# Performance work log

Hardware: AMD Instinct MI355X
Metric: run time of the kernel (lower is better)

Reference implementation:

```python
import jax, jax.numpy as jnp
import numpy as np

B, S, H = 4, 1024, 1024
NH, HD = 16, 64
SCALE = 1.0 / np.sqrt(HD)
VERB_BIAS, ROOT_BIAS, SUFFIX_BIAS = 2.0, 1.5, 1.2
BIG = np.float32(1e9)


def setup_inputs() -> dict:
    key = jax.random.key(0)
    ks = jax.random.split(key, 10)
    inp = {
        "hidden_states": jax.random.normal(ks[0], (B, S, H), dtype=jnp.float32),
        "morpho_types": jax.random.randint(ks[1], (B, S), 0, 5, dtype=jnp.int32),
        # torch Linear: y = x @ W.T + b; store W already transposed as [in, out]
        "Wq": jax.random.normal(ks[2], (H, H), dtype=jnp.float32) * 0.02,
        "bq": jnp.zeros((H,), dtype=jnp.float32),
        "Wk": jax.random.normal(ks[3], (H, H), dtype=jnp.float32) * 0.02,
        "bk": jnp.zeros((H,), dtype=jnp.float32),
        "Wv": jax.random.normal(ks[4], (H, H), dtype=jnp.float32) * 0.02,
        "bv": jnp.zeros((H,), dtype=jnp.float32),
        "Wo": jax.random.normal(ks[5], (H, H), dtype=jnp.float32) * 0.02,
        "bo": jnp.zeros((H,), dtype=jnp.float32),
    }
    return inp


def _morpho_bias(morpho_types):
    """Vectorized equivalent of _create_morpho_bias_mask. Returns [B, S, S]
    (the torch version broadcasts the same bias over all heads)."""
    is_verb = morpho_types == 2                      # [B, S]
    pos = jnp.arange(S)
    dist = jnp.abs(pos[:, None] - pos[None, :])      # [S, S]
    # mask non-verb columns with a huge distance; argmin ties -> smallest j,
    # matching torch's argmin over ascending verb_positions
    dist_m = jnp.where(is_verb[:, None, :], dist[None], BIG)  # [B, S, S]
    nearest = jnp.argmin(dist_m, axis=-1)            # [B, S]
    has_verb = jnp.any(is_verb, axis=-1)             # [B]
    verb_term = VERB_BIAS * jax.nn.one_hot(nearest, S, dtype=jnp.float32)
    verb_term = verb_term * has_verb[:, None, None].astype(jnp.float32)
    col_bias = (ROOT_BIAS * 0.5) * (morpho_types == 0).astype(jnp.float32) \
             + (SUFFIX_BIAS * 0.3) * (morpho_types == 1).astype(jnp.float32)  # [B, S]
    return verb_term + col_bias[:, None, :]          # [B, S, S]


def reference(hidden_states, morpho_types, Wq, bq, Wk, bk, Wv, bv, Wo, bo):
    def proj(W, b):
        y = hidden_states @ W + b                    # [B, S, H]
        return y.reshape(B, S, NH, HD).transpose(0, 2, 1, 3)  # [B, NH, S, HD]

    q = proj(Wq, bq)
    k = proj(Wk, bk)
    v = proj(Wv, bv)

    scores = jnp.einsum('bhqd,bhkd->bhqk', q, k) * SCALE   # [B, NH, S, S]
    scores = scores + _morpho_bias(morpho_types)[:, None]  # broadcast heads

    attn = jax.nn.softmax(scores, axis=-1)
    out = jnp.einsum('bhqk,bhkd->bhqd', attn, v)           # [B, NH, S, HD]
    out = out.transpose(0, 2, 1, 3).reshape(B, S, H)
    return out @ Wo + bo
```

## Files before the change

### kernel.cpp

```cpp
#include <hip/hip_runtime.h>


#define QSCALE 0.18033688011112042f
#define CB0    1.0820212806667225f
#define CB1    0.5193702147200268f
#define VERB2  2.8853900817779268f

typedef float  f32x4   __attribute__((ext_vector_type(4)));
typedef short  s16x8   __attribute__((ext_vector_type(8)));
typedef unsigned short u16x4 __attribute__((ext_vector_type(4)));
typedef unsigned short u16x8 __attribute__((ext_vector_type(8)));

#if __has_builtin(__builtin_amdgcn_exp2f)
#define EXP2F(x) __builtin_amdgcn_exp2f(x)
#else
#define EXP2F(x) exp2f(x)
#endif

__device__ __forceinline__ unsigned short f2bf(float f) {
  union { float f; unsigned u; } a; a.f = f;
  unsigned r = a.u + 0x7fffu + ((a.u >> 16) & 1u);
  return (unsigned short)(r >> 16);
}

__device__ __forceinline__ void async16(const void* g, void* l) {
  __builtin_amdgcn_global_load_lds(
      (const __attribute__((address_space(1))) unsigned int*)g,
      (__attribute__((address_space(3))) unsigned int*)l, 16, 0, 0);
}

__global__ __launch_bounds__(256) void k_prep(
    const float* __restrict__ hs, unsigned short* __restrict__ hsb,
    const float* __restrict__ Wq, const float* __restrict__ Wk,
    const float* __restrict__ Wv, const float* __restrict__ Wo,
    unsigned short* __restrict__ Wt, const int* __restrict__ mt,
    float* __restrict__ colbias, int* __restrict__ nearest) {
  __shared__ float t[64 * 68];
  int bx = blockIdx.x, tid = threadIdx.x;
  if (bx < 2048) {
    int i = (bx * 256 + tid) * 8;
    float4 v0 = *(const float4*)(hs + i);
    float4 v1 = *(const float4*)(hs + i + 4);
    u16x8 o;
    o[0] = f2bf(v0.x); o[1] = f2bf(v0.y); o[2] = f2bf(v0.z); o[3] = f2bf(v0.w);
    o[4] = f2bf(v1.x); o[5] = f2bf(v1.y); o[6] = f2bf(v1.z); o[7] = f2bf(v1.w);
    *(u16x8*)(hsb + i) = o;
  } else if (bx < 3072) {
    int w = (bx - 2048) >> 8, tt = (bx - 2048) & 255;
    const float* W = (w == 0) ? Wq : (w == 1) ? Wk : (w == 2) ? Wv : Wo;
    unsigned short* Wd = Wt + (size_t)w * 1048576;
    int n0 = (tt & 15) * 64, k0 = (tt >> 4) * 64;
    int r = tid >> 2, c0 = (tid & 3) * 16;
    const float* src = &W[(k0 + r) * 1024 + n0 + c0];
    float4 a0 = *(const float4*)(src + 0);
    float4 a1 = *(const float4*)(src + 4);
    float4 a2 = *(const float4*)(src + 8);
    float4 a3 = *(const float4*)(src + 12);
    *(float4*)&t[r * 68 + c0 + 0]  = a0;
    *(float4*)&t[r * 68 + c0 + 4]  = a1;
    *(float4*)&t[r * 68 + c0 + 8]  = a2;
    *(float4*)&t[r * 68 + c0 + 12] = a3;
    __syncthreads();
    u16x8 o0, o1;
#pragma unroll
    for (int j = 0; j < 8; j++) {
      o0[j] = f2bf(t[(c0 + j) * 68 + r]);
      o1[j] = f2bf(t[(c0 + 8 + j) * 68 + r]);
    }
    *(u16x8*)&Wd[(n0 + r) * 1024 + k0 + c0]     = o0;
    *(u16x8*)&Wd[(n0 + r) * 1024 + k0 + c0 + 8] = o1;
  } else {
    int i = bx - 3072;
    int b = i >> 2;
    int* sm = (int*)t;
    for (int j = tid; j < 1024; j += 256) sm[j] = mt[b * 1024 + j];
    __syncthreads();
    int q = (i & 3) * 256 + tid;
    int best = 1 << 30, bj = -1;
    for (int j = 0; j < 1024; ++j) {
      int d = (q > j) ? (q - j) : (j - q);
      int dd = (sm[j] == 2) ? d : (1 << 30);
      if (dd < best) { best = dd; bj = j; }
    }
    nearest[b * 1024 + q] = bj;
    int m = sm[q];
    colbias[b * 1024 + q] = CB0 * (m == 0) + CB1 * (m == 1);
  }
}

template <int MODE>
__global__ __launch_bounds__(256) void k_gemm(
    const unsigned short* __restrict__ A,
    const unsigned short* __restrict__ WtBase,
    const float* __restrict__ bias0, const float* __restrict__ bias1,
    const float* __restrict__ bias2,
    unsigned short* __restrict__ outB, unsigned short* __restrict__ outV,
    float* __restrict__ outF) {
  __shared__ unsigned short As[128 * 32];
  __shared__ unsigned short Bs[128 * 32];
  int tid = threadIdx.x, wid = tid >> 6, lane = tid & 63;
  int c = lane & 15, quad = lane >> 4;
  int m0 = blockIdx.y * 128;
  int wsel, n0;
  const unsigned short* Bt;
  const float* bias;
  if (MODE == 0) {
    wsel = blockIdx.x >> 3;
    n0 = (blockIdx.x & 7) * 128;
    Bt = WtBase + wsel * 1048576;
    bias = (wsel == 0) ? bias0 : ((wsel == 1) ? bias1 : bias2);
  } else {
    wsel = 0; n0 = blockIdx.x * 128; Bt = WtBase; bias = bias0;
  }
  int wm = (wid >> 1) * 64, wn = (wid & 1) * 64;
  const unsigned short* ga = A  + (m0 + wid * 32 + (lane >> 2)) * 1024 + (lane & 3) * 8;
  const unsigned short* gb = Bt + (n0 + wid * 32 + (lane >> 2)) * 1024 + (lane & 3) * 8;
  unsigned short* lA = &As[wid * 32 * 32];
  unsigned short* lB = &Bs[wid * 32 * 32];

  f32x4 acc[4][4];
#pragma unroll
  for (int i = 0; i < 4; i++)
#pragma unroll
    for (int j = 0; j < 4; j++) acc[i][j] = (f32x4){0.f, 0.f, 0.f, 0.f};

  for (int k0 = 0; k0 < 1024; k0 += 32) {
    async16(ga + k0,             lA);
    async16(ga + 16 * 1024 + k0, lA + 16 * 32);
    async16(gb + k0,             lB);
    async16(gb + 16 * 1024 + k0, lB + 16 * 32);
    __syncthreads();
    s16x8 af[4], bf[4];
#pragma unroll
    for (int i = 0; i < 4; i++) af[i] = *(const s16x8*)&As[(wm + i * 16 + c) * 32 + quad * 8];
#pragma unroll
    for (int j = 0; j < 4; j++) bf[j] = *(const s16x8*)&Bs[(wn + j * 16 + c) * 32 + quad * 8];
#pragma unroll
    for (int i = 0; i < 4; i++)
#pragma unroll
      for (int j = 0; j < 4; j++)
        acc[i][j] = __builtin_amdgcn_mfma_f32_16x16x32_bf16(af[i], bf[j], acc[i][j], 0, 0, 0);
    __syncthreads();
  }

  if (MODE == 1) {
#pragma unroll
    for (int j = 0; j < 4; j++) {
      int col = n0 + wn + j * 16 + c;
      float bv = bias[col];
#pragma unroll
      for (int i = 0; i < 4; i++) {
        int row = m0 + wm + i * 16 + quad * 4;
#pragma unroll
        for (int r = 0; r < 4; r++) outF[(row + r) * 1024 + col] = acc[i][j][r] + bv;
      }
    }
  } else if (wsel == 2) {
#pragma unroll
    for (int j = 0; j < 4; j++) {
      int col = n0 + wn + j * 16 + c;
      float bv = bias[col];
      int h = col >> 6, d = col & 63;
#pragma unroll
      for (int i = 0; i < 4; i++) {
        int row = m0 + wm + i * 16 + quad * 4;
        int bb = row >> 10, s = row & 1023;
        u16x4 pk;
#pragma unroll
        for (int r = 0; r < 4; r++) pk[r] = f2bf(acc[i][j][r] + bv);
        *(u16x4*)&outV[(size_t)(((bb * 16 + h) * 64 + d)) * 1024 + s] = pk;
      }
    }
  } else {
    float sc = (wsel == 0) ? QSCALE : 1.0f;
#pragma unroll
    for (int j = 0; j < 4; j++) {
      int col = n0 + wn + j * 16 + c;
      float bv = bias[col];
      int h = col >> 6, d = col & 63;
#pragma unroll
      for (int i = 0; i < 4; i++) {
        int row = m0 + wm + i * 16 + quad * 4;
#pragma unroll
        for (int r = 0; r < 4; r++) {
          int rr = row + r;
          int bb = rr >> 10, s = rr & 1023;
          outB[(size_t)wsel * 4194304 + (((bb * 16 + h) * 1024 + s) * 64) + d] =
              f2bf((acc[i][j][r] + bv) * sc);
        }
      }
    }
  }
}

__global__ __launch_bounds__(256) void k_attn(
    const unsigned short* __restrict__ Q, const unsigned short* __restrict__ K,
    const unsigned short* __restrict__ Vt, const float* __restrict__ colbias,
    const int* __restrict__ nearest, unsigned short* __restrict__ AO) {
  __shared__ unsigned short Ks[64 * 72];
  __shared__ unsigned short Vs[64 * 72];
  __shared__ unsigned short Ps[4][32 * 72];
  __shared__ float Cb[1024];
  int tid = threadIdx.x, wid = tid >> 6, lane = tid & 63;
  int c = lane & 15, quad = lane >> 4;
  int bh = blockIdx.x, qt = blockIdx.y;
  int b = bh >> 4, head = bh & 15;
  int q0 = qt * 128, wq = wid * 32;
  const unsigned short* Qg = Q  + (size_t)(bh * 1024 + q0 + wq) * 64;
  const unsigned short* Kg = K  + (size_t)bh * 1024 * 64;
  const unsigned short* Vg = Vt + (size_t)bh * 64 * 1024;

  *(float4*)&Cb[tid * 4] = *(const float4*)&colbias[b * 1024 + tid * 4];

  s16x8 qf[2][2];
#pragma unroll
  for (int nt = 0; nt < 2; nt++)
#pragma unroll
    for (int ks = 0; ks < 2; ks++)
      qf[nt][ks] = *(const s16x8*)&Qg[(nt * 16 + c) * 64 + ks * 32 + quad * 8];

  int nq[2];
  nq[0] = nearest[b * 1024 + q0 + wq + c];
  nq[1] = nearest[b * 1024 + q0 + wq + 16 + c];

  f32x4 o[2][4];
#pragma unroll
  for (int i = 0; i < 2; i++)
#pragma unroll
    for (int j = 0; j < 4; j++) o[i][j] = (f32x4){0.f, 0.f, 0.f, 0.f};
  float lrun[2] = {0.f, 0.f};

  int srow = tid >> 3, scol8 = (tid & 7) * 8;

  u16x8 kr[2], vr[2];
#pragma unroll
  for (int it = 0; it < 2; ++it) {
    int r2 = it * 32 + srow;
    kr[it] = *(const u16x8*)&Kg[r2 * 64 + scol8];
    vr[it] = *(const u16x8*)&Vg[r2 * 1024 + scol8];
  }
  __syncthreads();

  for (int kc = 0; kc < 16; ++kc) {
#pragma unroll
    for (int it = 0; it < 2; ++it) {
      int r2 = it * 32 + srow;
      *(u16x8*)&Ks[r2 * 72 + scol8] = kr[it];
      *(u16x8*)&Vs[r2 * 72 + scol8] = vr[it];
    }
    __syncthreads();
    if (kc < 15) {
#pragma unroll
      for (int it = 0; it < 2; ++it) {
        int r2 = it * 32 + srow;
        kr[it] = *(const u16x8*)&Kg[((kc + 1) * 64 + r2) * 64 + scol8];
        vr[it] = *(const u16x8*)&Vg[r2 * 1024 + (kc + 1) * 64 + scol8];
      }
    }

    f32x4 st[4][2];
#pragma unroll
    for (int mt = 0; mt < 4; mt++)
#pragma unroll
      for (int nt = 0; nt < 2; nt++) st[mt][nt] = (f32x4){0.f, 0.f, 0.f, 0.f};
#pragma unroll
    for (int mt = 0; mt < 4; mt++)
#pragma unroll
      for (int ks = 0; ks < 2; ks++) {
        s16x8 a = *(const s16x8*)&Ks[(mt * 16 + c) * 72 + ks * 32 + quad * 8];
#pragma unroll
        for (int nt = 0; nt < 2; nt++)
          st[mt][nt] = __builtin_amdgcn_mfma_f32_16x16x32_bf16(a, qf[nt][ks], st[mt][nt], 0, 0, 0);
      }

#pragma unroll
    for (int mt = 0; mt < 4; mt++) {
      f32x4 cb = *(const f32x4*)&Cb[kc * 64 + mt * 16 + quad * 4];
#pragma unroll
      for (int nt = 0; nt < 2; nt++) {
        u16x4 pk;
#pragma unroll
        for (int r = 0; r < 4; r++) {
          int keyg = kc * 64 + mt * 16 + quad * 4 + r;
          float x = st[mt][nt][r] + cb[r] + ((keyg == nq[nt]) ? VERB2 : 0.f);
          float e = EXP2F(x);
          lrun[nt] += e;
          pk[r] = f2bf(e);
        }
        *(u16x4*)&Ps[wid][(nt * 16 + c) * 72 + mt * 16 + quad * 4] = pk;
      }
    }
    __asm__ volatile("s_waitcnt lgkmcnt(0)" ::: "memory");

#pragma unroll
    for (int ks = 0; ks < 2; ks++) {
      s16x8 pa[2];
#pragma unroll
      for (int mtq = 0; mtq < 2; mtq++)
        pa[mtq] = *(const s16x8*)&Ps[wid][(mtq * 16 + c) * 72 + ks * 32 + quad * 8];
#pragma unroll
      for (int ntd = 0; ntd < 4; ntd++) {
        s16x8 vb = *(const s16x8*)&Vs[(ntd * 16 + c) * 72 + ks * 32 + quad * 8];
#pragma unroll
        for (int mtq = 0; mtq < 2; mtq++)
          o[mtq][ntd] = __builtin_amdgcn_mfma_f32_16x16x32_bf16(pa[mtq], vb, o[mtq][ntd], 0, 0, 0);
      }
    }
    __syncthreads();
  }

#pragma unroll
  for (int nt = 0; nt < 2; nt++) {
    lrun[nt] += __shfl_xor(lrun[nt], 16, 64);
    lrun[nt] += __shfl_xor(lrun[nt], 32, 64);
  }
  float linv[2] = {1.0f / lrun[0], 1.0f / lrun[1]};
#pragma unroll
  for (int mtq = 0; mtq < 2; mtq++)
#pragma unroll
    for (int r = 0; r < 4; r++) {
      float lq = __shfl(linv[mtq], quad * 4 + r, 64);
      size_t row = (size_t)(b * 1024 + q0 + wq + mtq * 16 + quad * 4 + r);
#pragma unroll
      for (int ntd = 0; ntd < 4; ntd++)
        AO[row * 1024 + head * 64 + ntd * 16 + c] = f2bf(o[mtq][ntd][r] * lq);
    }
}

extern "C" void kernel_launch(void* const* d_in, const int* in_sizes, int n_in,
                              void* d_out, int out_size, void* d_ws, size_t ws_size,
                              hipStream_t stream) {
  const float* hs     = (const float*)d_in[0];
  const int*   morpho = (const int*)d_in[1];
  const float* Wq = (const float*)d_in[2];
  const float* bq = (const float*)d_in[3];
  const float* Wk = (const float*)d_in[4];
  const float* bk = (const float*)d_in[5];
  const float* Wv = (const float*)d_in[6];
  const float* bv = (const float*)d_in[7];
  const float* Wo = (const float*)d_in[8];
  const float* bo = (const float*)d_in[9];
  float* out = (float*)d_out;

  char* ws = (char*)d_ws;
  unsigned short* hsb = (unsigned short*)(ws);
  unsigned short* Wt  = (unsigned short*)(ws + (8u << 20));
  unsigned short* Qb  = (unsigned short*)(ws + (16u << 20));
  unsigned short* Kb  = (unsigned short*)(ws + (24u << 20));
  unsigned short* Vtb = (unsigned short*)(ws + (40u << 20));
  float* colbias      = (float*)(ws + (48u << 20));
  int*   nearestp     = (int*)(ws + (48u << 20) + (16u << 10));
  unsigned short* AO  = hsb;

  k_prep<<<3088, 256, 0, stream>>>(hs, hsb, Wq, Wk, Wv, Wo, Wt, morpho,
                                   colbias, nearestp);
  k_gemm<0><<<dim3(24, 32), 256, 0, stream>>>(hsb, Wt, bq, bk, bv, Qb, Vtb, nullptr);
  k_attn<<<dim3(64, 8), 256, 0, stream>>>(Qb, Kb, Vtb, colbias, nearestp, AO);
  k_gemm<1><<<dim3(8, 32), 256, 0, stream>>>(AO, Wt + 3 * 1048576, bo, nullptr, nullptr,
                                             nullptr, nullptr, out);
  (void)in_sizes; (void)n_in; (void)out_size; (void)ws_size; (void)Kb;
}
```

Baseline: 231.5 us.

## Swap MFMA operands for vectorized epilogue stores and remap GEMM blocks per XCD

Operands of the MFMA instructions are swapped in the projection GEMMs and in the attention P·V product, so each lane holds four consecutive output columns. The epilogues can then issue 16-byte or 8-byte vector stores instead of scattered scalar stores. The GEMM grid is also remapped so that blocks sharing input rows are grouped per XCD, to improve L2 locality. This adds some index arithmetic and a branch on the weight selector inside the k-loop.

```diff
diff --git a/kernel.cpp b/kernel.cpp
--- a/kernel.cpp
+++ b/kernel.cpp
@@ -100,17 +100,24 @@
   __shared__ unsigned short Bs[128 * 32];
   int tid = threadIdx.x, wid = tid >> 6, lane = tid & 63;
   int c = lane & 15, quad = lane >> 4;
-  int m0 = blockIdx.y * 128;
-  int wsel, n0;
+  int m0, wsel, n0;
   const unsigned short* Bt;
   const float* bias;
   if (MODE == 0) {
-    wsel = blockIdx.x >> 3;
-    n0 = (blockIdx.x & 7) * 128;
+    int lin = blockIdx.x + 24 * blockIdx.y;
+    int xcd = lin & 7, idx = lin >> 3;
+    m0 = (((xcd >> 1) << 3) + (idx & 7)) * 128;
+    int xt = (xcd & 1) * 12 + (idx >> 3);
+    wsel = xt >> 3;
+    n0 = (xt & 7) * 128;
     Bt = WtBase + wsel * 1048576;
     bias = (wsel == 0) ? bias0 : ((wsel == 1) ? bias1 : bias2);
   } else {
-    wsel = 0; n0 = blockIdx.x * 128; Bt = WtBase; bias = bias0;
+    int lin = blockIdx.x + 8 * blockIdx.y;
+    int xcd = lin & 7, idx = lin >> 3;
+    m0 = ((xcd << 2) + (idx & 3)) * 128;
+    n0 = (idx >> 2) * 128;
+    wsel = 0; Bt = WtBase; bias = bias0;
   }
   int wm = (wid >> 1) * 64, wn = (wid & 1) * 64;
   const unsigned short* ga = A  + (m0 + wid * 32 + (lane >> 2)) * 1024 + (lane & 3) * 8;
@@ -124,6 +131,8 @@
 #pragma unroll
     for (int j = 0; j < 4; j++) acc[i][j] = (f32x4){0.f, 0.f, 0.f, 0.f};
 
+  bool sw = (MODE == 1) || (wsel != 2);
+
   for (int k0 = 0; k0 < 1024; k0 += 32) {
     async16(ga + k0,             lA);
     async16(ga + 16 * 1024 + k0, lA + 16 * 32);
@@ -135,24 +144,32 @@
     for (int i = 0; i < 4; i++) af[i] = *(const s16x8*)&As[(wm + i * 16 + c) * 32 + quad * 8];
 #pragma unroll
     for (int j = 0; j < 4; j++) bf[j] = *(const s16x8*)&Bs[(wn + j * 16 + c) * 32 + quad * 8];
-#pragma unroll
-    for (int i = 0; i < 4; i++)
-#pragma unroll
-      for (int j = 0; j < 4; j++)
-        acc[i][j] = __builtin_amdgcn_mfma_f32_16x16x32_bf16(af[i], bf[j], acc[i][j], 0, 0, 0);
+    if (sw) {
+#pragma unroll
+      for (int i = 0; i < 4; i++)
+#pragma unroll
+        for (int j = 0; j < 4; j++)
+          acc[i][j] = __builtin_amdgcn_mfma_f32_16x16x32_bf16(bf[j], af[i], acc[i][j], 0, 0, 0);
+    } else {
+#pragma unroll
+      for (int i = 0; i < 4; i++)
+#pragma unroll
+        for (int j = 0; j < 4; j++)
+          acc[i][j] = __builtin_amdgcn_mfma_f32_16x16x32_bf16(af[i], bf[j], acc[i][j], 0, 0, 0);
+    }
     __syncthreads();
   }
 
   if (MODE == 1) {
 #pragma unroll
     for (int j = 0; j < 4; j++) {
-      int col = n0 + wn + j * 16 + c;
-      float bv = bias[col];
+      int colb = n0 + wn + j * 16 + quad * 4;
+      f32x4 bvv = *(const f32x4*)&bias[colb];
 #pragma unroll
       for (int i = 0; i < 4; i++) {
-        int row = m0 + wm + i * 16 + quad * 4;
-#pragma unroll
-        for (int r = 0; r < 4; r++) outF[(row + r) * 1024 + col] = acc[i][j][r] + bv;
+        int s_tok = m0 + wm + i * 16 + c;
+        f32x4 v = acc[i][j] + bvv;
+        *(f32x4*)&outF[(size_t)s_tok * 1024 + colb] = v;
       }
     }
   } else if (wsel == 2) {
@@ -175,19 +192,17 @@
     float sc = (wsel == 0) ? QSCALE : 1.0f;
 #pragma unroll
     for (int j = 0; j < 4; j++) {
-      int col = n0 + wn + j * 16 + c;
-      float bv = bias[col];
-      int h = col >> 6, d = col & 63;
+      int colb = n0 + wn + j * 16 + quad * 4;
+      f32x4 bvv = *(const f32x4*)&bias[colb];
+      int h = colb >> 6, d0 = colb & 63;
 #pragma unroll
       for (int i = 0; i < 4; i++) {
-        int row = m0 + wm + i * 16 + quad * 4;
-#pragma unroll
-        for (int r = 0; r < 4; r++) {
-          int rr = row + r;
-          int bb = rr >> 10, s = rr & 1023;
-          outB[(size_t)wsel * 4194304 + (((bb * 16 + h) * 1024 + s) * 64) + d] =
-              f2bf((acc[i][j][r] + bv) * sc);
-        }
+        int s_tok = m0 + wm + i * 16 + c;
+        int bb = s_tok >> 10, s = s_tok & 1023;
+        u16x4 pk;
+#pragma unroll
+        for (int r = 0; r < 4; r++) pk[r] = f2bf((acc[i][j][r] + bvv[r]) * sc);
+        *(u16x4*)&outB[(size_t)wsel * 4194304 + (((bb * 16 + h) * 1024 + s) * 64) + d0] = pk;
       }
     }
   }
@@ -303,7 +318,7 @@
         s16x8 vb = *(const s16x8*)&Vs[(ntd * 16 + c) * 72 + ks * 32 + quad * 8];
 #pragma unroll
         for (int mtq = 0; mtq < 2; mtq++)
-          o[mtq][ntd] = __builtin_amdgcn_mfma_f32_16x16x32_bf16(pa[mtq], vb, o[mtq][ntd], 0, 0, 0);
+          o[mtq][ntd] = __builtin_amdgcn_mfma_f32_16x16x32_bf16(vb, pa[mtq], o[mtq][ntd], 0, 0, 0);
       }
     }
     __syncthreads();
@@ -316,15 +331,17 @@
   }
   float linv[2] = {1.0f / lrun[0], 1.0f / lrun[1]};
 #pragma unroll
-  for (int mtq = 0; mtq < 2; mtq++)
-#pragma unroll
-    for (int r = 0; r < 4; r++) {
-      float lq = __shfl(linv[mtq], quad * 4 + r, 64);
-      size_t row = (size_t)(b * 1024 + q0 + wq + mtq * 16 + quad * 4 + r);
-#pragma unroll
-      for (int ntd = 0; ntd < 4; ntd++)
-        AO[row * 1024 + head * 64 + ntd * 16 + c] = f2bf(o[mtq][ntd][r] * lq);
-    }
+  for (int mtq = 0; mtq < 2; mtq++) {
+    size_t row = (size_t)(b * 1024 + q0 + wq + mtq * 16 + c);
+#pragma unroll
+    for (int ntd = 0; ntd < 4; ntd++) {
+      int d0 = ntd * 16 + quad * 4;
+      u16x4 pk;
+#pragma unroll
+      for (int r = 0; r < 4; r++) pk[r] = f2bf(o[mtq][ntd][r] * linv[mtq]);
+      *(u16x4*)&AO[row * 1024 + head * 64 + d0] = pk;
+    }
+  }
 }
 
 extern "C" void kernel_launch(void* const* d_in, const int* in_sizes, int n_in,
```

New measurement: 229.8 us. About the same (-0.8%).
